# Kernel optimization log

Measured on AMD Instinct MI355X. Metric: run time of the kernel, lower is better.

The kernel has to match this reference:

```python
import jax, jax.numpy as jnp
import numpy as np

N = 16384      # number of nodes
F_IN = 64      # input feature dim
F_OUT = 64     # out_dim


def setup_inputs() -> dict:
    key = jax.random.key(0)
    k1, k2, k3 = jax.random.split(key, 3)
    inp = jax.random.normal(k1, (N, F_IN), dtype=jnp.float32)
    adj = jax.random.uniform(k2, (N, N), dtype=jnp.float32)
    # Dense(out_dim, use_bias=False) kernel, glorot-uniform-ish init
    limit = np.sqrt(6.0 / (F_IN + F_OUT)).astype(np.float32)
    W = jax.random.uniform(k3, (F_IN, F_OUT), dtype=jnp.float32, minval=-limit, maxval=limit)
    b = jnp.zeros((F_OUT,), dtype=jnp.float32)  # gcn_b, zeros init
    return {"input": inp, "adj": adj, "W": W, "b": b}


def reference(input, adj, W, b):
    # x = Dense(x) ; x = adj @ x ; x += b
    h = input @ W                  # [N, F_out]
    out = adj @ h + b              # [N, F_out]
    return out
```

## Files before the change

### kernel.cpp

```cpp
#include <hip/hip_runtime.h>
#include <hip/hip_bf16.h>
#include <stdint.h>

typedef __attribute__((ext_vector_type(4))) float f32x4;
typedef __attribute__((ext_vector_type(8))) __bf16 bf16x8;
typedef __attribute__((ext_vector_type(2))) unsigned int u32x2;
typedef __attribute__((ext_vector_type(4))) unsigned int u32x4;

#define N_NODES 16384
#define F_DIM   64

__device__ inline unsigned cvtpk_bf16(float lo, float hi) {
    unsigned r;
    asm("v_cvt_pk_bf16_f32 %0, %1, %2" : "=v"(r) : "v"(lo), "v"(hi));
    return r;
}

__global__ __launch_bounds__(256) void dense_h(const float* __restrict__ inp,
                                               const float* __restrict__ W,
                                               short* __restrict__ hpack) {
    __shared__ float in_lds[64][64];
    __shared__ float wt_lds[64][68];
    const int t = threadIdx.x;
    const int blk = blockIdx.x;

#pragma unroll
    for (int i = 0; i < 4; ++i) {
        int n = i * 256 + t; int row = n >> 4; int c = n & 15;
        f32x4 v = *(const f32x4*)(inp + (size_t)(blk * 64 + row) * 64 + c * 4);
        *(f32x4*)(&in_lds[row][c * 4]) = v;
    }
#pragma unroll
    for (int i = 0; i < 4; ++i) {
        int n = i * 256 + t; int k = n >> 4; int c = n & 15;
        f32x4 v = *(const f32x4*)(W + k * 64 + c * 4);
        wt_lds[c * 4 + 0][k] = v.x; wt_lds[c * 4 + 1][k] = v.y;
        wt_lds[c * 4 + 2][k] = v.z; wt_lds[c * 4 + 3][k] = v.w;
    }
    __syncthreads();

#pragma unroll
    for (int cc = 0; cc < 2; ++cc) {
        int c = cc * 256 + t;
        int kbL = c >> 8; int ct = (c >> 6) & 3; int l = c & 63;
        int f  = ct * 16 + (l & 15);
        int r0 = kbL * 32 + (l >> 4) * 8;
        float acc[8] = {0, 0, 0, 0, 0, 0, 0, 0};
        for (int k = 0; k < 64; k += 4) {
            f32x4 wv = *(const f32x4*)(&wt_lds[f][k]);
#pragma unroll
            for (int j = 0; j < 8; ++j) {
                f32x4 iv = *(const f32x4*)(&in_lds[r0 + j][k]);
                acc[j] += iv.x * wv.x + iv.y * wv.y + iv.z * wv.z + iv.w * wv.w;
            }
        }
        u32x4 w4 = {cvtpk_bf16(acc[0], acc[1]), cvtpk_bf16(acc[2], acc[3]),
                    cvtpk_bf16(acc[4], acc[5]), cvtpk_bf16(acc[6], acc[7])};
        int kb = blk * 2 + kbL;
        *(u32x4*)(hpack + ((size_t)(kb * 4 + ct) * 64 + l) * 8) = w4;
    }
}

__global__ __launch_bounds__(256, 2) void spmm_adj(const float* __restrict__ adj,
                                                   const short* __restrict__ hp,
                                                   float* __restrict__ out,
                                                   int kspan) {
    const int rb = blockIdx.x;
    const int sp = blockIdx.y;
    const int k0 = sp * kspan;
    const int iters = kspan >> 6;
    const int t  = threadIdx.x;
    const int wv = t >> 6;
    const int ln = t & 63;

    __shared__ short At[2][64 * 64];

    const size_t rowbase = (size_t)(rb * 64) * N_NODES;

    auto ldA = [&](int tt, f32x4* rv) {
        const float* base = adj + rowbase + (size_t)(k0 + tt * 64);
#pragma unroll
        for (int i = 0; i < 4; ++i) {
            int row = i * 16 + (t >> 4); int c = t & 15;
            rv[i] = __builtin_nontemporal_load((const f32x4*)(base + (size_t)row * N_NODES + c * 4));
        }
    };
    auto stA = [&](int buf, const f32x4* rv) {
#pragma unroll
        for (int i = 0; i < 4; ++i) {
            int row = i * 16 + (t >> 4); int c = t & 15;
            u32x2 w = {cvtpk_bf16(rv[i].x, rv[i].y), cvtpk_bf16(rv[i].z, rv[i].w)};
            int byte = row * 128 + ((c * 8) ^ ((row & 7) << 4));
            *(u32x2*)((char*)At[buf] + byte) = w;
        }
    };
    auto ldB = [&](int tt, bf16x8* b) {
        const short* h = hp + (size_t)(k0 >> 5) * 2048 + (size_t)tt * 4096 + ln * 8;
#pragma unroll
        for (int ks2 = 0; ks2 < 2; ++ks2)
#pragma unroll
            for (int ct = 0; ct < 4; ++ct)
                b[ks2 * 4 + ct] = *(const bf16x8*)(h + ks2 * 2048 + ct * 512);
    };

    f32x4 acc[4] = {{0,0,0,0},{0,0,0,0},{0,0,0,0},{0,0,0,0}};
    const int abase = (wv * 16 + (ln & 15)) * 128;
    const int axor  = (ln & 7) << 4;
    const int koff  = (ln >> 4) * 16;

    auto mfmaPhase = [&](int buf, const bf16x8* b) {
#pragma unroll
        for (int ks2 = 0; ks2 < 2; ++ks2) {
            bf16x8 a = *(const bf16x8*)((const char*)At[buf] + abase + ((ks2 * 64 + koff) ^ axor));
#pragma unroll
            for (int ct = 0; ct < 4; ++ct)
                acc[ct] = __builtin_amdgcn_mfma_f32_16x16x32_bf16(a, b[ks2 * 4 + ct], acc[ct], 0, 0, 0);
        }
    };

    f32x4 rvA[4], rvB[4];
    bf16x8 bbA[8], bbB[8];

    ldB(0, bbA);
    ldA(0, rvA);
    ldB(1, bbB);
    ldA(1, rvB);
    stA(0, rvA);
    asm volatile("s_waitcnt lgkmcnt(0)" ::: "memory");
    __builtin_amdgcn_s_barrier();

    int tt = 0;
    for (; tt + 2 < iters; tt += 2) {
        mfmaPhase(0, bbA);
        ldB(tt + 2, bbA);
        ldA(tt + 2, rvA);
        __builtin_amdgcn_sched_barrier(0);
        stA(1, rvB);
        asm volatile("s_waitcnt lgkmcnt(0)" ::: "memory");
        __builtin_amdgcn_s_barrier();
        mfmaPhase(1, bbB);
        ldB(tt + 3, bbB);
        ldA(tt + 3, rvB);
        __builtin_amdgcn_sched_barrier(0);
        stA(0, rvA);
        asm volatile("s_waitcnt lgkmcnt(0)" ::: "memory");
        __builtin_amdgcn_s_barrier();
    }
    mfmaPhase(0, bbA);
    stA(1, rvB);
    asm volatile("s_waitcnt lgkmcnt(0)" ::: "memory");
    __builtin_amdgcn_s_barrier();
    mfmaPhase(1, bbB);

    float* o = out + (size_t)sp * ((size_t)N_NODES * F_DIM);
    const int orow0 = rb * 64 + wv * 16 + (ln >> 4) * 4;
    const int col   = ln & 15;
#pragma unroll
    for (int ct = 0; ct < 4; ++ct)
#pragma unroll
        for (int j = 0; j < 4; ++j)
            o[(size_t)(orow0 + j) * F_DIM + ct * 16 + col] = acc[ct][j];
}

__global__ __launch_bounds__(256) void reduce_add(const float* __restrict__ part,
                                                  const float* __restrict__ bias,
                                                  float* __restrict__ out, int nsp) {
    int g = blockIdx.x * 256 + threadIdx.x;
    f32x4 s = {0, 0, 0, 0};
    for (int i = 0; i < nsp; ++i)
        s += *(const f32x4*)(part + (size_t)i * ((size_t)N_NODES * F_DIM) + (size_t)g * 4);
    f32x4 bv = *(const f32x4*)(bias + ((g * 4) & 63));
    *(f32x4*)(out + (size_t)g * 4) = s + bv;
}

extern "C" void kernel_launch(void* const* d_in, const int* in_sizes, int n_in,
                              void* d_out, int out_size, void* d_ws, size_t ws_size,
                              hipStream_t stream) {
    const float* inp = (const float*)d_in[0];
    const float* adj = (const float*)d_in[1];
    const float* W   = (const float*)d_in[2];
    const float* b   = (const float*)d_in[3];
    float* out = (float*)d_out;

    char*  ws = (char*)d_ws;
    const size_t HP = (size_t)N_NODES * F_DIM * sizeof(short);
    short* hpack = (short*)ws;
    float* partial = (float*)(ws + HP);
    const size_t P1 = (size_t)N_NODES * F_DIM * sizeof(float);

    dense_h<<<N_NODES / 64, 256, 0, stream>>>(inp, W, hpack);

    if (ws_size >= HP + 4 * P1) {
        dim3 g(N_NODES / 64, 4);
        spmm_adj<<<g, 256, 0, stream>>>(adj, hpack, partial, N_NODES / 4);
        reduce_add<<<(N_NODES * F_DIM) / 1024, 256, 0, stream>>>(partial, b, out, 4);
    } else if (ws_size >= HP + P1) {
        dim3 g(N_NODES / 64, 1);
        spmm_adj<<<g, 256, 0, stream>>>(adj, hpack, partial, N_NODES);
        reduce_add<<<(N_NODES * F_DIM) / 1024, 256, 0, stream>>>(partial, b, out, 1);
    } else {
        dim3 g(N_NODES / 64, 1);
        spmm_adj<<<g, 256, 0, stream>>>(adj, hpack, out, N_NODES);
        reduce_add<<<(N_NODES * F_DIM) / 1024, 256, 0, stream>>>(out, b, out, 1);
    }
}
```

Baseline: 229.4 us.

## Give each wave private LDS A-tiles and drop block barriers in spmm loop

Each wave now loads and converts only its own 16 rows of adj into a per-wave LDS buffer, so the block-wide s_barrier and explicit waitcnt between pipeline stages are removed. The register double-buffering is replaced with a single set of A and B registers, and launch bounds are raised to 4 blocks per SIMD to get more occupancy to hide memory latency. The nontemporal load hint on adj is dropped. Per-wave rows are now 16 scattered 256-byte segments per load rather than block-coalesced tiles, and less explicit prefetch depth puts more reliance on occupancy.

New measurement: 239.3 us. 1.04x slower.

```diff
diff --git a/kernel.cpp b/kernel.cpp
--- a/kernel.cpp
+++ b/kernel.cpp
@@ -61,7 +61,7 @@
     }
 }
 
-__global__ __launch_bounds__(256, 2) void spmm_adj(const float* __restrict__ adj,
+__global__ __launch_bounds__(256, 4) void spmm_adj(const float* __restrict__ adj,
                                                    const short* __restrict__ hp,
                                                    float* __restrict__ out,
                                                    int kspan) {
@@ -73,29 +73,28 @@
     const int wv = t >> 6;
     const int ln = t & 63;
 
-    __shared__ short At[2][64 * 64];
+    __shared__ short At[4][2][16 * 64];
 
-    const size_t rowbase = (size_t)(rb * 64) * N_NODES;
+    const int lr = ln >> 4;
+    const int lc = ln & 15;
+    const float* baseA = adj + (size_t)(rb * 64 + wv * 16) * N_NODES + k0 + lc * 4;
 
     auto ldA = [&](int tt, f32x4* rv) {
-        const float* base = adj + rowbase + (size_t)(k0 + tt * 64);
+#pragma unroll
+        for (int i = 0; i < 4; ++i)
+            rv[i] = *(const f32x4*)(baseA + (size_t)(i * 4 + lr) * N_NODES + tt * 64);
+    };
+    auto stA = [&](int buf, const f32x4* rv) {
+        char* base = (char*)At[wv][buf];
 #pragma unroll
         for (int i = 0; i < 4; ++i) {
-            int row = i * 16 + (t >> 4); int c = t & 15;
-            rv[i] = __builtin_nontemporal_load((const f32x4*)(base + (size_t)row * N_NODES + c * 4));
-        }
-    };
-    auto stA = [&](int buf, const f32x4* rv) {
-#pragma unroll
-        for (int i = 0; i < 4; ++i) {
-            int row = i * 16 + (t >> 4); int c = t & 15;
+            int r = i * 4 + lr;
             u32x2 w = {cvtpk_bf16(rv[i].x, rv[i].y), cvtpk_bf16(rv[i].z, rv[i].w)};
-            int byte = row * 128 + ((c * 8) ^ ((row & 7) << 4));
-            *(u32x2*)((char*)At[buf] + byte) = w;
+            *(u32x2*)(base + r * 128 + ((lc * 8) ^ ((r & 7) << 4))) = w;
         }
     };
     auto ldB = [&](int tt, bf16x8* b) {
-        const short* h = hp + (size_t)(k0 >> 5) * 2048 + (size_t)tt * 4096 + ln * 8;
+        const short* h = hp + ((size_t)(k0 >> 5) + tt * 2) * 2048 + ln * 8;
 #pragma unroll
         for (int ks2 = 0; ks2 < 2; ++ks2)
 #pragma unroll
@@ -104,53 +103,47 @@
     };
 
     f32x4 acc[4] = {{0,0,0,0},{0,0,0,0},{0,0,0,0},{0,0,0,0}};
-    const int abase = (wv * 16 + (ln & 15)) * 128;
-    const int axor  = (ln & 7) << 4;
+    const int abase = (ln & 15) * 128;
+    const int aswz  = (ln & 7) << 4;
     const int koff  = (ln >> 4) * 16;
 
     auto mfmaPhase = [&](int buf, const bf16x8* b) {
+        const char* base = (const char*)At[wv][buf];
 #pragma unroll
         for (int ks2 = 0; ks2 < 2; ++ks2) {
-            bf16x8 a = *(const bf16x8*)((const char*)At[buf] + abase + ((ks2 * 64 + koff) ^ axor));
+            bf16x8 a = *(const bf16x8*)(base + abase + ((ks2 * 64 + koff) ^ aswz));
 #pragma unroll
             for (int ct = 0; ct < 4; ++ct)
                 acc[ct] = __builtin_amdgcn_mfma_f32_16x16x32_bf16(a, b[ks2 * 4 + ct], acc[ct], 0, 0, 0);
         }
     };
 
-    f32x4 rvA[4], rvB[4];
-    bf16x8 bbA[8], bbB[8];
+    f32x4 rv[4];
+    bf16x8 bb[8];
 
-    ldB(0, bbA);
-    ldA(0, rvA);
-    ldB(1, bbB);
-    ldA(1, rvB);
-    stA(0, rvA);
-    asm volatile("s_waitcnt lgkmcnt(0)" ::: "memory");
-    __builtin_amdgcn_s_barrier();
+    ldA(0, rv);
+    ldB(0, bb);
+    stA(0, rv);
 
     int tt = 0;
     for (; tt + 2 < iters; tt += 2) {
-        mfmaPhase(0, bbA);
-        ldB(tt + 2, bbA);
-        ldA(tt + 2, rvA);
+        ldA(tt + 1, rv);
         __builtin_amdgcn_sched_barrier(0);
-        stA(1, rvB);
-        asm volatile("s_waitcnt lgkmcnt(0)" ::: "memory");
-        __builtin_amdgcn_s_barrier();
-        mfmaPhase(1, bbB);
-        ldB(tt + 3, bbB);
-        ldA(tt + 3, rvB);
+        mfmaPhase(0, bb);
+        ldB(tt + 1, bb);
+        stA(1, rv);
+        ldA(tt + 2, rv);
         __builtin_amdgcn_sched_barrier(0);
-        stA(0, rvA);
-        asm volatile("s_waitcnt lgkmcnt(0)" ::: "memory");
-        __builtin_amdgcn_s_barrier();
+        mfmaPhase(1, bb);
+        ldB(tt + 2, bb);
+        stA(0, rv);
     }
-    mfmaPhase(0, bbA);
-    stA(1, rvB);
-    asm volatile("s_waitcnt lgkmcnt(0)" ::: "memory");
-    __builtin_amdgcn_s_barrier();
-    mfmaPhase(1, bbB);
+    ldA(tt + 1, rv);
+    __builtin_amdgcn_sched_barrier(0);
+    mfmaPhase(0, bb);
+    ldB(tt + 1, bb);
+    stA(1, rv);
+    mfmaPhase(1, bb);
 
     float* o = out + (size_t)sp * ((size_t)N_NODES * F_DIM);
     const int orow0 = rb * 64 + wv * 16 + (ln >> 4) * 4;
```
